# Optimization experiments

Measured on AMD Instinct MI355X. Metric: run time of the kernel, lower is better.

The kernel has to match this reference:

```python
import jax, jax.numpy as jnp
import numpy as np

D_MODEL = 512
D_K = 64
D_V = 64
N_HEADS = 8
N = 4096
EPS = 1e-5


def setup_inputs() -> dict:
    key = jax.random.key(0)
    ks = jax.random.split(key, 12)
    s = 1.0 / np.sqrt(D_MODEL)
    return {
        "Q": jax.random.normal(ks[0], (N, D_MODEL), dtype=jnp.float32),
        "K": jax.random.normal(ks[1], (N, D_MODEL), dtype=jnp.float32),
        "V": jax.random.normal(ks[2], (N, D_MODEL), dtype=jnp.float32),
        "W_Q": jax.random.normal(ks[3], (D_K * N_HEADS, D_MODEL), dtype=jnp.float32) * s,
        "b_Q": jnp.zeros((D_K * N_HEADS,), jnp.float32),
        "W_K": jax.random.normal(ks[4], (D_K * N_HEADS, D_MODEL), dtype=jnp.float32) * s,
        "b_K": jnp.zeros((D_K * N_HEADS,), jnp.float32),
        "W_V": jax.random.normal(ks[5], (D_V * N_HEADS, D_MODEL), dtype=jnp.float32) * s,
        "b_V": jnp.zeros((D_V * N_HEADS,), jnp.float32),
        "W_O": jax.random.normal(ks[6], (D_MODEL, N_HEADS * D_V), dtype=jnp.float32) * s,
        "b_O": jnp.zeros((D_MODEL,), jnp.float32),
        "gamma": jnp.ones((D_MODEL,), jnp.float32),
        "beta": jnp.zeros((D_MODEL,), jnp.float32),
    }


def reference(Q, K, V, W_Q, b_Q, W_K, b_K, W_V, b_V, W_O, b_O, gamma, beta):
    n = Q.shape[0]
    # projections (torch Linear: x @ W.T + b), then split heads: [N, H, dk]
    Qs = (Q @ W_Q.T + b_Q).reshape(n, N_HEADS, D_K)
    Ks = (K @ W_K.T + b_K).reshape(n, N_HEADS, D_K)
    Vs = (V @ W_V.T + b_V).reshape(n, N_HEADS, D_V)
    # per-head scaled dot-product attention over the N dim, batched via einsum
    scores = jnp.einsum("nhd,mhd->hnm", Qs, Ks) / np.sqrt(D_K)  # [H, N, N]
    attn = jax.nn.softmax(scores, axis=-1)
    ctx = jnp.einsum("hnm,mhd->nhd", attn, Vs)  # [N, H, dv]
    context = ctx.reshape(n, N_HEADS * D_V)  # concat heads (matches torch.cat order)
    out = context @ W_O.T + b_O + Q  # output proj + residual
    # LayerNorm over last dim
    mu = jnp.mean(out, axis=-1, keepdims=True)
    var = jnp.mean((out - mu) ** 2, axis=-1, keepdims=True)
    return (out - mu) * jax.lax.rsqrt(var + EPS) * gamma + beta
```

## Files before the change

### kernel.cpp

```cpp
#include <hip/hip_runtime.h>
#include <cstdint>

#define N_TOK 4096
#define DMODEL 512
#define NHEADS 8
#define HDIM 64

typedef unsigned short u16;
typedef __bf16 bf16x8 __attribute__((ext_vector_type(8)));
typedef float f32x4 __attribute__((ext_vector_type(4)));

union U128 { uint4 u; bf16x8 b; u16 s[8]; };

__device__ __forceinline__ u16 f2bf(float f) {
  uint32_t u = __builtin_bit_cast(uint32_t, f);
  u += 0x7FFFu + ((u >> 16) & 1u);
  return (u16)(u >> 16);
}
__device__ __forceinline__ float bf2f(u16 s) {
  uint32_t u = ((uint32_t)s) << 16;
  return __builtin_bit_cast(float, u);
}

#if __has_builtin(__builtin_amdgcn_exp2f)
#define EXP2(x) __builtin_amdgcn_exp2f(x)
#else
#define EXP2(x) __expf((x) * 0.6931471805599453f)
#endif

__device__ __forceinline__ uint32_t cvtpk(float lo, float hi) {
  uint32_t r;
  asm("v_cvt_pk_bf16_f32 %0, %1, %2" : "=v"(r) : "v"(lo), "v"(hi));
  return r;
}

__device__ __forceinline__ void ldg2lds16(const void* g, void* s) {
  __builtin_amdgcn_global_load_lds(
      (const __attribute__((address_space(1))) void*)g,
      (__attribute__((address_space(3))) void*)s, 16, 0, 0);
}

__global__ __launch_bounds__(256) void cvt7_kernel(
    const float* __restrict__ Q, const float* __restrict__ K, const float* __restrict__ V,
    const float* __restrict__ WQ, const float* __restrict__ WK, const float* __restrict__ WV,
    const float* __restrict__ WO,
    u16* __restrict__ Qb, u16* __restrict__ Kb, u16* __restrict__ Vb,
    u16* __restrict__ WQb, u16* __restrict__ WKb, u16* __restrict__ WVb,
    u16* __restrict__ WOb)
{
  int b = blockIdx.x;
  const float* src; u16* dst; int rel;
  if      (b < 2048) { src = Q;  dst = Qb;  rel = b; }
  else if (b < 4096) { src = K;  dst = Kb;  rel = b - 2048; }
  else if (b < 6144) { src = V;  dst = Vb;  rel = b - 4096; }
  else if (b < 6400) { src = WQ; dst = WQb; rel = b - 6144; }
  else if (b < 6656) { src = WK; dst = WKb; rel = b - 6400; }
  else if (b < 6912) { src = WV; dst = WVb; rel = b - 6656; }
  else               { src = WO; dst = WOb; rel = b - 6912; }
  int i = (rel * 256 + threadIdx.x) * 4;
  float4 f = *(const float4*)(src + i);
  ushort4 o;
  o.x = f2bf(f.x); o.y = f2bf(f.y); o.z = f2bf(f.z); o.w = f2bf(f.w);
  *(ushort4*)(dst + i) = o;
}

__global__ __launch_bounds__(256) void proj3_kernel(
    const u16* __restrict__ Qb, const u16* __restrict__ Kb, const u16* __restrict__ Vb,
    const u16* __restrict__ WQb, const u16* __restrict__ WKb, const u16* __restrict__ WVb,
    const float* __restrict__ bQ, const float* __restrict__ bK, const float* __restrict__ bV,
    u16* __restrict__ Qs, u16* __restrict__ Ks, u16* __restrict__ Vt)
{
  const int z = blockIdx.z;
  const u16* A      = (z == 0) ? Qb : (z == 1) ? Kb : Vb;
  const u16* W      = (z == 0) ? WQb : (z == 1) ? WKb : WVb;
  const float* bias = (z == 0) ? bQ : (z == 1) ? bK : bV;

  const int m0 = blockIdx.x * 128;
  const int j0 = blockIdx.y * 64;
  const int tid = threadIdx.x;
  const int w = tid >> 6, lane = tid & 63, quad = lane >> 4, l = lane & 15;

  __shared__ bf16x8 sA[2][8][128];
  __shared__ bf16x8 sB[2][8][64];

  const f32x4 zero = {0.f, 0.f, 0.f, 0.f};
  f32x4 acc[2][4];
#pragma unroll
  for (int m = 0; m < 2; ++m)
#pragma unroll
    for (int s = 0; s < 4; ++s) acc[m][s] = zero;

  auto stage = [&](int kt, int buf) {
    const int k0 = kt * 64;
#pragma unroll
    for (int i = 0; i < 4; ++i) {
      const int chunk = 2 * w + (i >> 1), half = (i & 1) * 64;
      const u16* ag = A + (size_t)(m0 + half + lane) * DMODEL + k0 + chunk * 8;
      ldg2lds16(ag, (char*)&sA[buf][chunk][half]);
    }
#pragma unroll
    for (int i = 0; i < 2; ++i) {
      const int chunk = 2 * w + i;
      const u16* bg = W + (size_t)(j0 + lane) * DMODEL + k0 + chunk * 8;
      ldg2lds16(bg, (char*)&sB[buf][chunk][0]);
    }
  };

  stage(0, 0);
  __syncthreads();
  for (int kt = 0; kt < 8; ++kt) {
    const int buf = kt & 1;
    if (kt + 1 < 8) stage(kt + 1, buf ^ 1);
#pragma unroll
    for (int c = 0; c < 2; ++c) {
      bf16x8 af0 = sA[buf][c * 4 + quad][w * 32 + l];
      bf16x8 af1 = sA[buf][c * 4 + quad][w * 32 + 16 + l];
#pragma unroll
      for (int s = 0; s < 4; ++s) {
        bf16x8 bfb = sB[buf][c * 4 + quad][s * 16 + l];
        acc[0][s] = __builtin_amdgcn_mfma_f32_16x16x32_bf16(af0, bfb, acc[0][s], 0, 0, 0);
        acc[1][s] = __builtin_amdgcn_mfma_f32_16x16x32_bf16(af1, bfb, acc[1][s], 0, 0, 0);
      }
    }
    __syncthreads();
  }

#pragma unroll
  for (int m = 0; m < 2; ++m)
#pragma unroll
    for (int s = 0; s < 4; ++s) {
      int j = j0 + s * 16 + l;
      float bv = bias[j];
      int n0 = m0 + w * 32 + m * 16 + quad * 4;
      if (z < 2) {
        u16* Y = (z == 0) ? Qs : Ks;
#pragma unroll
        for (int r = 0; r < 4; ++r)
          Y[(size_t)(n0 + r) * DMODEL + j] = f2bf(acc[m][s][r] + bv);
      } else {
        ushort4 pk;
        pk.x = f2bf(acc[m][s][0] + bv); pk.y = f2bf(acc[m][s][1] + bv);
        pk.z = f2bf(acc[m][s][2] + bv); pk.w = f2bf(acc[m][s][3] + bv);
        *(ushort4*)(Vt + (size_t)j * N_TOK + n0) = pk;
      }
    }
}

__global__ __launch_bounds__(512, 4) void attn_kernel(
    const u16* __restrict__ Qs, const u16* __restrict__ Ks,
    const u16* __restrict__ Vt, u16* __restrict__ Opart, float* __restrict__ Lpart)
{
  const int hs = blockIdx.x;
  const int h = hs & 7, split = hs >> 3;
  const int qt = blockIdx.y;
  const int tid = threadIdx.x;
  const int w = tid >> 6, lane = tid & 63, quad = lane >> 4, l = lane & 15;

  __shared__ bf16x8 kch[2][8][64];
  __shared__ bf16x8 vch[2][8][64];
  __shared__ __align__(128) u16 pbuf[8][32][64];

  const int wq0 = qt * 256 + w * 32;

  bf16x8 qf[2][2];
#pragma unroll
  for (int c = 0; c < 2; ++c)
#pragma unroll
    for (int m = 0; m < 2; ++m) {
      U128 u;
      u.u = *(const uint4*)(Qs + (size_t)(wq0 + m * 16 + l) * DMODEL + h * HDIM + c * 32 + quad * 8);
#pragma unroll
      for (int j = 0; j < 8; ++j) u.s[j] = f2bf(bf2f(u.s[j]) * 0.18033688f);
      qf[c][m] = u.b;
    }

  U128 onesu;
#pragma unroll
  for (int j = 0; j < 8; ++j) onesu.s[j] = 0x3F80;

  const f32x4 zero = {0.f, 0.f, 0.f, 0.f};
  f32x4 o[2][4];
  f32x4 ol[2];
  ol[0] = zero; ol[1] = zero;
#pragma unroll
  for (int m = 0; m < 2; ++m)
#pragma unroll
    for (int s = 0; s < 4; ++s) o[m][s] = zero;

  auto stage = [&](int it, int buf) {
    const int j0 = split * 1024 + it * 64;
    if (w < 4) {
      const u16* kg = Ks + (size_t)(j0 + lane) * DMODEL + h * HDIM + w * 16;
      ldg2lds16(kg,     (char*)&kch[buf][2 * w][0]);
      ldg2lds16(kg + 8, (char*)&kch[buf][2 * w + 1][0]);
    } else {
      const int w2 = w - 4;
      const u16* vg = Vt + (size_t)(h * HDIM + lane) * N_TOK + j0 + w2 * 16;
      ldg2lds16(vg,     (char*)&vch[buf][2 * w2][0]);
      ldg2lds16(vg + 8, (char*)&vch[buf][2 * w2 + 1][0]);
    }
  };

  stage(0, 0);
  __syncthreads();

  const unsigned swz = (unsigned)((l & 7) << 4);

  for (int it = 0; it < 16; ++it) {
    const int buf = it & 1;
    if (it + 1 < 16) stage(it + 1, buf ^ 1);

#pragma unroll
    for (int kh = 0; kh < 2; ++kh) {
#pragma unroll
      for (int tt = 0; tt < 2; ++tt) {
        const int t = kh * 2 + tt;
        f32x4 sacc[2];
        sacc[0] = zero; sacc[1] = zero;
#pragma unroll
        for (int c = 0; c < 2; ++c) {
          bf16x8 kf = kch[buf][c * 4 + quad][t * 16 + l];
          sacc[0] = __builtin_amdgcn_mfma_f32_16x16x32_bf16(kf, qf[c][0], sacc[0], 0, 0, 0);
          sacc[1] = __builtin_amdgcn_mfma_f32_16x16x32_bf16(kf, qf[c][1], sacc[1], 0, 0, 0);
        }
#pragma unroll
        for (int m = 0; m < 2; ++m) {
          uint2 st;
          st.x = cvtpk(EXP2(sacc[m][0]), EXP2(sacc[m][1]));
          st.y = cvtpk(EXP2(sacc[m][2]), EXP2(sacc[m][3]));
          char* pb = (char*)&pbuf[w][m * 16 + l][0];
          *(uint2*)(pb + (((unsigned)(tt * 32 + quad * 8)) ^ swz)) = st;
        }
      }
      U128 pf0, pf1;
      const unsigned ro = ((unsigned)(quad * 16)) ^ swz;
      pf0.u = *(const uint4*)((const char*)&pbuf[w][l][0] + ro);
      pf1.u = *(const uint4*)((const char*)&pbuf[w][16 + l][0] + ro);
#pragma unroll
      for (int s = 0; s < 4; ++s) {
        bf16x8 vf = vch[buf][kh * 4 + quad][s * 16 + l];
        o[0][s] = __builtin_amdgcn_mfma_f32_16x16x32_bf16(pf0.b, vf, o[0][s], 0, 0, 0);
        o[1][s] = __builtin_amdgcn_mfma_f32_16x16x32_bf16(pf1.b, vf, o[1][s], 0, 0, 0);
      }
      ol[0] = __builtin_amdgcn_mfma_f32_16x16x32_bf16(pf0.b, onesu.b, ol[0], 0, 0, 0);
      ol[1] = __builtin_amdgcn_mfma_f32_16x16x32_bf16(pf1.b, onesu.b, ol[1], 0, 0, 0);
    }
    __syncthreads();
  }

  if (l == 0) {
    float* Lp = Lpart + ((size_t)split * NHEADS + h) * N_TOK + wq0;
#pragma unroll
    for (int m = 0; m < 2; ++m)
#pragma unroll
      for (int r = 0; r < 4; ++r)
        Lp[m * 16 + quad * 4 + r] = ol[m][r];
  }
  u16* Ob = Opart + ((size_t)(split * NHEADS + h) * N_TOK + wq0) * 64;
#pragma unroll
  for (int m = 0; m < 2; ++m)
#pragma unroll
    for (int s = 0; s < 4; ++s)
#pragma unroll
      for (int r = 0; r < 4; ++r)
        Ob[(size_t)(m * 16 + quad * 4 + r) * 64 + s * 16 + l] = f2bf(o[m][s][r]);
}

__global__ __launch_bounds__(1024) void outfuse_kernel(
    const u16* __restrict__ Opart, const float* __restrict__ Lpart,
    const u16* __restrict__ WOb, const float* __restrict__ bO,
    const float* __restrict__ resid, const float* __restrict__ gamma,
    const float* __restrict__ beta, float* __restrict__ Y)
{
  __shared__ __align__(128) char smem[16384 + 2 * 65536];
  bf16x8* sA = (bf16x8*)smem;
  bf16x8* sB = (bf16x8*)(smem + 16384);
  float* pls = (float*)smem;
  float* plq = (float*)smem + 256;
  float* mrow = (float*)smem + 512;

  const int tid = threadIdx.x;
  const int w = tid >> 6, lane = tid & 63, quad = lane >> 4, l = lane & 15;
  const int n0 = blockIdx.x * 16;

  auto stageB = [&](int kt, int buf) {
#pragma unroll
    for (int t = 0; t < 4; ++t) {
      const int jb = w * 32 + t * 8;
      const u16* g = WOb + (size_t)(jb + (lane >> 3)) * DMODEL + kt * 64
                   + (((lane & 7) ^ (lane >> 3)) * 8);
      ldg2lds16(g, (char*)&sB[(size_t)buf * 4096 + jb * 8]);
    }
  };

  stageB(0, 0);

  {
    const int h = tid >> 7;
    const int n = (tid >> 3) & 15;
    const int vd0 = (tid & 7) * 8;
    float a8[8] = {0, 0, 0, 0, 0, 0, 0, 0};
    float lsum = 0.f;
#pragma unroll
    for (int s = 0; s < 4; ++s) {
      U128 u;
      u.u = *(const uint4*)(Opart + ((size_t)(s * NHEADS + h) * N_TOK + n0 + n) * 64 + vd0);
#pragma unroll
      for (int j = 0; j < 8; ++j) a8[j] += bf2f(u.s[j]);
      lsum += Lpart[((size_t)s * NHEADS + h) * N_TOK + n0 + n];
    }
    float inv = 1.f / lsum;
    U128 o;
#pragma unroll
    for (int j = 0; j < 8; ++j) o.s[j] = f2bf(a8[j] * inv);
    const int col8 = h * 8 + (tid & 7);
    *(uint4*)&sA[col8 * 16 + n] = o.u;
  }
  __syncthreads();

  const f32x4 zero = {0.f, 0.f, 0.f, 0.f};
  f32x4 acc[2];
  acc[0] = zero; acc[1] = zero;

  for (int kt = 0; kt < 8; ++kt) {
    const int buf = kt & 1;
    if (kt + 1 < 8) stageB(kt + 1, buf ^ 1);
#pragma unroll
    for (int c = 0; c < 2; ++c) {
      bf16x8 af = sA[(kt * 8 + c * 4 + quad) * 16 + l];
#pragma unroll
      for (int s = 0; s < 2; ++s) {
        const int j = w * 32 + s * 16 + l;
        bf16x8 bfb = sB[(size_t)buf * 4096 + j * 8 + ((c * 4 + quad) ^ (l & 7))];
        acc[s] = __builtin_amdgcn_mfma_f32_16x16x32_bf16(af, bfb, acc[s], 0, 0, 0);
      }
    }
    __syncthreads();
  }

  float vb[2][4];
#pragma unroll
  for (int s = 0; s < 2; ++s) {
    const int j = w * 32 + s * 16 + l;
    const float bv = bO[j];
#pragma unroll
    for (int r = 0; r < 4; ++r)
      vb[s][r] = acc[s][r] + bv + resid[(size_t)(n0 + quad * 4 + r) * DMODEL + j];
  }
#pragma unroll
  for (int r = 0; r < 4; ++r) {
    float sm = vb[0][r] + vb[1][r];
    float sq = vb[0][r] * vb[0][r] + vb[1][r] * vb[1][r];
#pragma unroll
    for (int mk = 1; mk < 16; mk <<= 1) {
      sm += __shfl_xor(sm, mk);
      sq += __shfl_xor(sq, mk);
    }
    if (l == 0) {
      pls[(quad * 4 + r) * 16 + w] = sm;
      plq[(quad * 4 + r) * 16 + w] = sq;
    }
  }
  __syncthreads();
  if (tid < 16) {
    float sm = 0.f, sq = 0.f;
#pragma unroll
    for (int w2 = 0; w2 < 16; ++w2) { sm += pls[tid * 16 + w2]; sq += plq[tid * 16 + w2]; }
    const float mu = sm * (1.f / DMODEL);
    const float var = sq * (1.f / DMODEL) - mu * mu;
    mrow[tid * 2]     = mu;
    mrow[tid * 2 + 1] = rsqrtf(var + 1e-5f);
  }
  __syncthreads();
#pragma unroll
  for (int s = 0; s < 2; ++s) {
    const int j = w * 32 + s * 16 + l;
    const float gj = gamma[j], bj = beta[j];
#pragma unroll
    for (int r = 0; r < 4; ++r) {
      const int row = quad * 4 + r;
      const float mu = mrow[row * 2], sc = mrow[row * 2 + 1];
      Y[(size_t)(n0 + row) * DMODEL + j] = (vb[s][r] - mu) * sc * gj + bj;
    }
  }
}

extern "C" void kernel_launch(void* const* d_in, const int* in_sizes, int n_in,
                              void* d_out, int out_size, void* d_ws, size_t ws_size,
                              hipStream_t stream)
{
  const float* Q     = (const float*)d_in[0];
  const float* K     = (const float*)d_in[1];
  const float* V     = (const float*)d_in[2];
  const float* WQ    = (const float*)d_in[3];
  const float* bQ    = (const float*)d_in[4];
  const float* WK    = (const float*)d_in[5];
  const float* bK    = (const float*)d_in[6];
  const float* WV    = (const float*)d_in[7];
  const float* bV    = (const float*)d_in[8];
  const float* WO    = (const float*)d_in[9];
  const float* bO    = (const float*)d_in[10];
  const float* gamma = (const float*)d_in[11];
  const float* beta  = (const float*)d_in[12];

  const size_t MB = 1ull << 20;
  char* ws = (char*)d_ws;
  u16* Qb   = (u16*)(ws + 0 * MB);
  u16* Kb   = (u16*)(ws + 4 * MB);
  u16* Vb   = (u16*)(ws + 8 * MB);
  u16* WQb  = (u16*)(ws + 12 * MB);
  u16* WKb  = (u16*)(ws + 12 * MB + 512 * 1024);
  u16* WVb  = (u16*)(ws + 13 * MB);
  u16* WOb  = (u16*)(ws + 13 * MB + 512 * 1024);
  u16* Qs   = (u16*)(ws + 14 * MB);
  u16* Ks   = (u16*)(ws + 18 * MB);
  u16* Vt   = (u16*)(ws + 22 * MB);
  u16* Opart = (u16*)(ws + 30 * MB);
  float* Lpart = (float*)(ws + 46 * MB);
  float* out = (float*)d_out;

  cvt7_kernel<<<7168, 256, 0, stream>>>(Q, K, V, WQ, WK, WV, WO,
                                        Qb, Kb, Vb, WQb, WKb, WVb, WOb);
  proj3_kernel<<<dim3(32, 8, 3), 256, 0, stream>>>(Qb, Kb, Vb, WQb, WKb, WVb,
                                                   bQ, bK, bV, Qs, Ks, Vt);
  attn_kernel<<<dim3(32, 16), 512, 0, stream>>>(Qs, Ks, Vt, Opart, Lpart);
  outfuse_kernel<<<256, 1024, 0, stream>>>(Opart, Lpart, WOb, bO, Q,
                                           gamma, beta, out);
}
```

Measured before the change: 172.7 us.

## Fuse fp32-to-bf16 conversion into projection and output GEMM staging

```diff
diff --git a/kernel.cpp b/kernel.cpp
--- a/kernel.cpp
+++ b/kernel.cpp
@@ -33,6 +33,12 @@
   asm("v_cvt_pk_bf16_f32 %0, %1, %2" : "=v"(r) : "v"(lo), "v"(hi));
   return r;
 }
+__device__ __forceinline__ uint4 pack8(const float4& a, const float4& b) {
+  uint4 p;
+  p.x = cvtpk(a.x, a.y); p.y = cvtpk(a.z, a.w);
+  p.z = cvtpk(b.x, b.y); p.w = cvtpk(b.z, b.w);
+  return p;
+}
 
 __device__ __forceinline__ void ldg2lds16(const void* g, void* s) {
   __builtin_amdgcn_global_load_lds(
@@ -40,39 +46,15 @@
       (__attribute__((address_space(3))) void*)s, 16, 0, 0);
 }
 
-__global__ __launch_bounds__(256) void cvt7_kernel(
-    const float* __restrict__ Q, const float* __restrict__ K, const float* __restrict__ V,
+__global__ __launch_bounds__(256) void proj3_kernel(
+    const float* __restrict__ Qf, const float* __restrict__ Kf, const float* __restrict__ Vf,
     const float* __restrict__ WQ, const float* __restrict__ WK, const float* __restrict__ WV,
-    const float* __restrict__ WO,
-    u16* __restrict__ Qb, u16* __restrict__ Kb, u16* __restrict__ Vb,
-    u16* __restrict__ WQb, u16* __restrict__ WKb, u16* __restrict__ WVb,
-    u16* __restrict__ WOb)
-{
-  int b = blockIdx.x;
-  const float* src; u16* dst; int rel;
-  if      (b < 2048) { src = Q;  dst = Qb;  rel = b; }
-  else if (b < 4096) { src = K;  dst = Kb;  rel = b - 2048; }
-  else if (b < 6144) { src = V;  dst = Vb;  rel = b - 4096; }
-  else if (b < 6400) { src = WQ; dst = WQb; rel = b - 6144; }
-  else if (b < 6656) { src = WK; dst = WKb; rel = b - 6400; }
-  else if (b < 6912) { src = WV; dst = WVb; rel = b - 6656; }
-  else               { src = WO; dst = WOb; rel = b - 6912; }
-  int i = (rel * 256 + threadIdx.x) * 4;
-  float4 f = *(const float4*)(src + i);
-  ushort4 o;
-  o.x = f2bf(f.x); o.y = f2bf(f.y); o.z = f2bf(f.z); o.w = f2bf(f.w);
-  *(ushort4*)(dst + i) = o;
-}
-
-__global__ __launch_bounds__(256) void proj3_kernel(
-    const u16* __restrict__ Qb, const u16* __restrict__ Kb, const u16* __restrict__ Vb,
-    const u16* __restrict__ WQb, const u16* __restrict__ WKb, const u16* __restrict__ WVb,
     const float* __restrict__ bQ, const float* __restrict__ bK, const float* __restrict__ bV,
     u16* __restrict__ Qs, u16* __restrict__ Ks, u16* __restrict__ Vt)
 {
   const int z = blockIdx.z;
-  const u16* A      = (z == 0) ? Qb : (z == 1) ? Kb : Vb;
-  const u16* W      = (z == 0) ? WQb : (z == 1) ? WKb : WVb;
+  const float* A    = (z == 0) ? Qf : (z == 1) ? Kf : Vf;
+  const float* W    = (z == 0) ? WQ : (z == 1) ? WK : WV;
   const float* bias = (z == 0) ? bQ : (z == 1) ? bK : bV;
 
   const int m0 = blockIdx.x * 128;
@@ -90,27 +72,44 @@
 #pragma unroll
     for (int s = 0; s < 4; ++s) acc[m][s] = zero;
 
-  auto stage = [&](int kt, int buf) {
+  float4 fa[4][2], fb[2][2];
+
+  auto stage_load = [&](int kt) {
     const int k0 = kt * 64;
 #pragma unroll
     for (int i = 0; i < 4; ++i) {
       const int chunk = 2 * w + (i >> 1), half = (i & 1) * 64;
-      const u16* ag = A + (size_t)(m0 + half + lane) * DMODEL + k0 + chunk * 8;
-      ldg2lds16(ag, (char*)&sA[buf][chunk][half]);
+      const float* ag = A + (size_t)(m0 + half + lane) * DMODEL + k0 + chunk * 8;
+      fa[i][0] = *(const float4*)ag;
+      fa[i][1] = *(const float4*)(ag + 4);
     }
 #pragma unroll
     for (int i = 0; i < 2; ++i) {
       const int chunk = 2 * w + i;
-      const u16* bg = W + (size_t)(j0 + lane) * DMODEL + k0 + chunk * 8;
-      ldg2lds16(bg, (char*)&sB[buf][chunk][0]);
+      const float* bg = W + (size_t)(j0 + lane) * DMODEL + k0 + chunk * 8;
+      fb[i][0] = *(const float4*)bg;
+      fb[i][1] = *(const float4*)(bg + 4);
     }
   };
-
-  stage(0, 0);
+  auto stage_write = [&](int buf) {
+#pragma unroll
+    for (int i = 0; i < 4; ++i) {
+      const int chunk = 2 * w + (i >> 1), half = (i & 1) * 64;
+      *(uint4*)&sA[buf][chunk][half + lane] = pack8(fa[i][0], fa[i][1]);
+    }
+#pragma unroll
+    for (int i = 0; i < 2; ++i) {
+      const int chunk = 2 * w + i;
+      *(uint4*)&sB[buf][chunk][lane] = pack8(fb[i][0], fb[i][1]);
+    }
+  };
+
+  stage_load(0);
+  stage_write(0);
   __syncthreads();
   for (int kt = 0; kt < 8; ++kt) {
     const int buf = kt & 1;
-    if (kt + 1 < 8) stage(kt + 1, buf ^ 1);
+    if (kt + 1 < 8) stage_load(kt + 1);
 #pragma unroll
     for (int c = 0; c < 2; ++c) {
       bf16x8 af0 = sA[buf][c * 4 + quad][w * 32 + l];
@@ -122,6 +121,7 @@
         acc[1][s] = __builtin_amdgcn_mfma_f32_16x16x32_bf16(af1, bfb, acc[1][s], 0, 0, 0);
       }
     }
+    if (kt + 1 < 8) stage_write(buf ^ 1);
     __syncthreads();
   }
 
@@ -268,7 +268,7 @@
 
 __global__ __launch_bounds__(1024) void outfuse_kernel(
     const u16* __restrict__ Opart, const float* __restrict__ Lpart,
-    const u16* __restrict__ WOb, const float* __restrict__ bO,
+    const float* __restrict__ WO, const float* __restrict__ bO,
     const float* __restrict__ resid, const float* __restrict__ gamma,
     const float* __restrict__ beta, float* __restrict__ Y)
 {
@@ -283,17 +283,26 @@
   const int w = tid >> 6, lane = tid & 63, quad = lane >> 4, l = lane & 15;
   const int n0 = blockIdx.x * 16;
 
-  auto stageB = [&](int kt, int buf) {
+  float4 fw[4][2];
+  auto stageB_load = [&](int kt) {
 #pragma unroll
     for (int t = 0; t < 4; ++t) {
       const int jb = w * 32 + t * 8;
-      const u16* g = WOb + (size_t)(jb + (lane >> 3)) * DMODEL + kt * 64
-                   + (((lane & 7) ^ (lane >> 3)) * 8);
-      ldg2lds16(g, (char*)&sB[(size_t)buf * 4096 + jb * 8]);
+      const float* g = WO + (size_t)(jb + (lane >> 3)) * DMODEL + kt * 64
+                     + (((lane & 7) ^ (lane >> 3)) * 8);
+      fw[t][0] = *(const float4*)g;
+      fw[t][1] = *(const float4*)(g + 4);
     }
   };
-
-  stageB(0, 0);
+  auto stageB_write = [&](int buf) {
+#pragma unroll
+    for (int t = 0; t < 4; ++t) {
+      const int jb = w * 32 + t * 8;
+      *(uint4*)&sB[(size_t)buf * 4096 + jb * 8 + lane] = pack8(fw[t][0], fw[t][1]);
+    }
+  };
+
+  stageB_load(0);
 
   {
     const int h = tid >> 7;
@@ -316,6 +325,7 @@
     const int col8 = h * 8 + (tid & 7);
     *(uint4*)&sA[col8 * 16 + n] = o.u;
   }
+  stageB_write(0);
   __syncthreads();
 
   const f32x4 zero = {0.f, 0.f, 0.f, 0.f};
@@ -324,7 +334,7 @@
 
   for (int kt = 0; kt < 8; ++kt) {
     const int buf = kt & 1;
-    if (kt + 1 < 8) stageB(kt + 1, buf ^ 1);
+    if (kt + 1 < 8) stageB_load(kt + 1);
 #pragma unroll
     for (int c = 0; c < 2; ++c) {
       bf16x8 af = sA[(kt * 8 + c * 4 + quad) * 16 + l];
@@ -335,6 +345,7 @@
         acc[s] = __builtin_amdgcn_mfma_f32_16x16x32_bf16(af, bfb, acc[s], 0, 0, 0);
       }
     }
+    if (kt + 1 < 8) stageB_write(buf ^ 1);
     __syncthreads();
   }
 
@@ -405,25 +416,16 @@
 
   const size_t MB = 1ull << 20;
   char* ws = (char*)d_ws;
-  u16* Qb   = (u16*)(ws + 0 * MB);
-  u16* Kb   = (u16*)(ws + 4 * MB);
-  u16* Vb   = (u16*)(ws + 8 * MB);
-  u16* WQb  = (u16*)(ws + 12 * MB);
-  u16* WKb  = (u16*)(ws + 12 * MB + 512 * 1024);
-  u16* WVb  = (u16*)(ws + 13 * MB);
-  u16* WOb  = (u16*)(ws + 13 * MB + 512 * 1024);
-  u16* Qs   = (u16*)(ws + 14 * MB);
-  u16* Ks   = (u16*)(ws + 18 * MB);
-  u16* Vt   = (u16*)(ws + 22 * MB);
-  u16* Opart = (u16*)(ws + 30 * MB);
-  float* Lpart = (float*)(ws + 46 * MB);
+  u16* Qs   = (u16*)(ws + 0 * MB);
+  u16* Ks   = (u16*)(ws + 4 * MB);
+  u16* Vt   = (u16*)(ws + 8 * MB);
+  u16* Opart = (u16*)(ws + 12 * MB);
+  float* Lpart = (float*)(ws + 28 * MB);
   float* out = (float*)d_out;
 
-  cvt7_kernel<<<7168, 256, 0, stream>>>(Q, K, V, WQ, WK, WV, WO,
-                                        Qb, Kb, Vb, WQb, WKb, WVb, WOb);
-  proj3_kernel<<<dim3(32, 8, 3), 256, 0, stream>>>(Qb, Kb, Vb, WQb, WKb, WVb,
+  proj3_kernel<<<dim3(32, 8, 3), 256, 0, stream>>>(Q, K, V, WQ, WK, WV,
                                                    bQ, bK, bV, Qs, Ks, Vt);
   attn_kernel<<<dim3(32, 16), 512, 0, stream>>>(Qs, Ks, Vt, Opart, Lpart);
-  outfuse_kernel<<<256, 1024, 0, stream>>>(Opart, Lpart, WOb, bO, Q,
+  outfuse_kernel<<<256, 1024, 0, stream>>>(Opart, Lpart, WO, bO, Q,
                                            gamma, beta, out);
 }
```

Result: slower. 186.8 us (+8.2%).
